# Optimization experiments

Measured on AMD Instinct MI355X. Metric: run time of the kernel, lower is better.

## Reference

```python
import jax, jax.numpy as jnp
import numpy as np

B, IN_DIM, OUT_DIM, W_DIM, K, H, W = 16, 512, 512, 512, 3, 64, 64
LEAK = 0.2

def setup_inputs() -> dict:
    key = jax.random.key(0)
    ks = jax.random.split(key, 8)
    imgs = jax.random.normal(ks[0], (B, IN_DIM, H, W), dtype=jnp.float32)
    w_embs = jax.random.normal(ks[1], (B, W_DIM), dtype=jnp.float32)
    noise = jax.random.normal(ks[2], (B, 1, H, W), dtype=jnp.float32)
    # learned params (kaiming-ish scaling)
    conv_w = jax.random.normal(ks[3], (OUT_DIM, IN_DIM, K, K), dtype=jnp.float32) / np.sqrt(IN_DIM * K * K)
    conv_b = jax.random.normal(ks[4], (OUT_DIM,), dtype=jnp.float32) * 0.01
    style_w = jax.random.normal(ks[5], (IN_DIM, W_DIM), dtype=jnp.float32) / np.sqrt(W_DIM)
    style_b = jax.random.normal(ks[6], (IN_DIM,), dtype=jnp.float32) * 0.01
    noise_weight = jnp.float32(0.1)
    return {"imgs": imgs, "w_embs": w_embs, "noise": noise,
            "conv_w": conv_w, "conv_b": conv_b,
            "style_w": style_w, "style_b": style_b,
            "noise_weight": noise_weight}

def reference(imgs, w_embs, noise, conv_w, conv_b, style_w, style_b, noise_weight):
    # style modulation: [b, in_dim], +1 as in the torch code
    style = w_embs @ style_w.T + style_b + 1.0
    # per-sample modulated weight: [b, out, in, ky, kx]
    weight = conv_w[None] * style[:, None, :, None, None]
    # demodulation: L2 norm over (in, ky, kx)
    norm = jnp.sqrt(jnp.sum(weight * weight, axis=(2, 3, 4), keepdims=True))
    weight = weight / norm
    # grouped conv trick == vmap of per-sample conv with SAME padding
    def conv_one(x, w):  # x: [c,h,w], w: [out,in,ky,kx]
        return jax.lax.conv_general_dilated(
            x[None], w, window_strides=(1, 1), padding='SAME',
            dimension_numbers=('NCHW', 'OIHW', 'NCHW'))[0]
    out = jax.vmap(conv_one)(imgs, weight)  # [b, out, h, w]
    out = out + conv_b[None, :, None, None] + noise * noise_weight
    # LeakyReLU(0.2)
    return jnp.where(out >= 0, out, LEAK * out)
```

## Files before the change

### kernel.cpp

```cpp
#include <hip/hip_runtime.h>
#include <hip/hip_bf16.h>

#define B_    16
#define CI    512
#define CO    512
#define HH    64
#define WW    64
#define NPIX  4096
#define KTAPS 9
#define KTOT  (CI * KTAPS)
#define LEAK  0.2f

#define PY 66
#define PX 66
#define IMGPAD_ELEMS ((size_t)B_ * PY * PX * CI)

typedef __attribute__((ext_vector_type(8))) __bf16  bf16x8;
typedef __attribute__((ext_vector_type(4))) float   floatx4;

__device__ __forceinline__ void load_lds16(const __bf16* g, __bf16* l) {
    __builtin_amdgcn_global_load_lds(
        (const __attribute__((address_space(1))) unsigned int*)g,
        (__attribute__((address_space(3))) unsigned int*)(unsigned int)(uintptr_t)l,
        16, 0, 0);
}


__global__ void style_kernel(const float* __restrict__ w_embs,
                             const float* __restrict__ style_w,
                             const float* __restrict__ style_b,
                             float* __restrict__ style) {
    int b = blockIdx.y;
    int i = blockIdx.x * 256 + threadIdx.x;
    const float4* we = (const float4*)(w_embs + (size_t)b * 512);
    const float4* sw = (const float4*)(style_w + (size_t)i * 512);
    float acc = 0.f;
    #pragma unroll 8
    for (int k = 0; k < 128; ++k) {
        float4 a = we[k], c = sw[k];
        acc += a.x * c.x + a.y * c.y + a.z * c.z + a.w * c.w;
    }
    style[b * 512 + i] = acc + style_b[i] + 1.0f;
}

__global__ void w2_kernel(const float* __restrict__ conv_w, float* __restrict__ w2) {
    int idx = blockIdx.x * 256 + threadIdx.x;
    const float* p = conv_w + (size_t)idx * 9;
    float s = 0.f;
    #pragma unroll
    for (int t = 0; t < 9; ++t) s += p[t] * p[t];
    w2[idx] = s;
}

__global__ void invn_kernel(const float* __restrict__ w2,
                            const float* __restrict__ style,
                            float* __restrict__ invn) {
    __shared__ float st2[512];
    int b = blockIdx.y;
    int o = blockIdx.x * 256 + threadIdx.x;
    for (int i = threadIdx.x; i < 512; i += 256) {
        float s = style[b * 512 + i];
        st2[i] = s * s;
    }
    __syncthreads();
    const float* wr = w2 + (size_t)o * 512;
    float acc = 0.f;
    #pragma unroll 8
    for (int i = 0; i < 512; ++i) acc += wr[i] * st2[i];
    invn[b * 512 + o] = 1.0f / sqrtf(acc);
}

__global__ void wsh_kernel(const float* __restrict__ conv_w,
                           __bf16* __restrict__ wsh) {
    int o = blockIdx.x * 4 + (threadIdx.x >> 6);
    int i0 = (threadIdx.x & 63) * 8;
    const float* p = conv_w + ((size_t)o * 512 + i0) * 9;
    float w[8][9];
    #pragma unroll
    for (int j = 0; j < 8; ++j)
        #pragma unroll
        for (int t = 0; t < 9; ++t) w[j][t] = p[j * 9 + t];
    __bf16* dstB = wsh + (size_t)o * KTOT + i0;
    #pragma unroll
    for (int t = 0; t < 9; ++t) {
        bf16x8 v;
        #pragma unroll
        for (int j = 0; j < 8; ++j) v[j] = (__bf16)w[j][t];
        *(bf16x8*)(dstB + t * 512) = v;
    }
}

__global__ void halo_kernel(__bf16* __restrict__ imgpad) {
    int t = blockIdx.x * 256 + threadIdx.x;
    if (t >= B_ * 260 * 64) return;
    int c8 = t & 63;
    int rest = t >> 6;
    int px = rest % 260;
    int b = rest / 260;
    int y, x;
    if (px < 66)       { y = 0;  x = px; }
    else if (px < 132) { y = 65; x = px - 66; }
    else { int s = px - 132; y = 1 + (s >> 1); x = (s & 1) * 65; }
    float4 z = {0.f, 0.f, 0.f, 0.f};
    *(float4*)&imgpad[(((size_t)b * PY + y) * PX + x) * 512 + c8 * 8] = z;
}

__global__ void imgpad_kernel(const float* __restrict__ imgs,
                              const float* __restrict__ style,
                              __bf16* __restrict__ imgpad) {
    __shared__ float tile[64][65];
    int ic = blockIdx.x, h = blockIdx.y, b = blockIdx.z;
    int t = threadIdx.x;
    int i0 = ic * 64;
    {
        int li = t >> 2;
        int w0 = (t & 3) * 16;
        const float* src = imgs + (((size_t)(b * 512 + i0 + li) * 64 + h) * 64 + w0);
        float4 v0 = ((const float4*)src)[0];
        float4 v1 = ((const float4*)src)[1];
        float4 v2 = ((const float4*)src)[2];
        float4 v3 = ((const float4*)src)[3];
        tile[li][w0 +  0] = v0.x; tile[li][w0 +  1] = v0.y;
        tile[li][w0 +  2] = v0.z; tile[li][w0 +  3] = v0.w;
        tile[li][w0 +  4] = v1.x; tile[li][w0 +  5] = v1.y;
        tile[li][w0 +  6] = v1.z; tile[li][w0 +  7] = v1.w;
        tile[li][w0 +  8] = v2.x; tile[li][w0 +  9] = v2.y;
        tile[li][w0 + 10] = v2.z; tile[li][w0 + 11] = v2.w;
        tile[li][w0 + 12] = v3.x; tile[li][w0 + 13] = v3.y;
        tile[li][w0 + 14] = v3.z; tile[li][w0 + 15] = v3.w;
    }
    __syncthreads();
    {
        int c0 = (t & 7) * 8;
        float st[8];
        #pragma unroll
        for (int j = 0; j < 8; ++j) st[j] = style[b * 512 + i0 + c0 + j];
        #pragma unroll
        for (int g = 0; g < 2; ++g) {
            int w = (t >> 3) + g * 32;
            bf16x8 v;
            #pragma unroll
            for (int j = 0; j < 8; ++j) v[j] = (__bf16)(tile[c0 + j][w] * st[j]);
            __bf16* dst = imgpad + (((size_t)b * PY + (h + 1)) * PX + (w + 1)) * 512 + i0 + c0;
            *(bf16x8*)dst = v;
        }
    }
}


#define BM 256
#define BN 256
#define BK 64
#define NT 72

#define BAR() { __builtin_amdgcn_sched_barrier(0);                            \
                __builtin_amdgcn_s_barrier();                                 \
                __builtin_amdgcn_sched_barrier(0); }

#define RA(PTR, BUFL, MI) (*(const bf16x8*)((PTR) + (BUFL) * 32768 + (MI) * 2048))
#define RB(PTR, BUFL, NI) (*(const bf16x8*)((PTR) + (BUFL) * 32768 + (NI) * 2048))

#define DSTA(BUFL, H, J) (&As[BUFL][(((H) * 128 + (J) * 64) + (wv << 3)) * 64])
#define DSTB(BUFL, H, J) (&Bs[BUFL][(((H) * 128 + (J) * 64) + (wv << 3)) * 64])

#define MFMA_PH(Q)                                                            \
    __builtin_amdgcn_s_setprio(1);                                            \
    _Pragma("unroll") for (int e = 0; e < 2; ++e) {                           \
      _Pragma("unroll") for (int ni = 0; ni < 4; ++ni) {                      \
        acc[2*(Q)+e][ni] = __builtin_amdgcn_mfma_f32_16x16x32_bf16(           \
            af[e][0], bf[ni][0], acc[2*(Q)+e][ni], 0, 0, 0);                  \
        acc[2*(Q)+e][ni] = __builtin_amdgcn_mfma_f32_16x16x32_bf16(           \
            af[e][1], bf[ni][1], acc[2*(Q)+e][ni], 0, 0, 0);                  \
      }                                                                       \
    }                                                                         \
    __builtin_amdgcn_s_setprio(0);

#define TILE(BUF, T, DO_A, DO_B, VME) {                                       \
                          \
    _Pragma("unroll") for (int ni = 0; ni < 4; ++ni) {                        \
        bf[ni][0] = RB(ldsB0, BUF, ni); bf[ni][1] = RB(ldsB1, BUF, ni);       \
    }                                                                         \
    af[0][0] = RA(ldsA0, BUF, 0); af[0][1] = RA(ldsA1, BUF, 0);               \
    af[1][0] = RA(ldsA0, BUF, 1); af[1][1] = RA(ldsA1, BUF, 1);               \
    if (DO_A) { int ka = ((T) + 1) * 64;                                      \
        load_lds16(aG00 + ka, DSTA((BUF) ^ 1, 0, 0));                         \
        load_lds16(aG01 + ka, DSTA((BUF) ^ 1, 0, 1)); }                       \
    MFMA_PH(0)                                                                \
                                        \
    af[0][0] = RA(ldsA0, BUF, 2); af[0][1] = RA(ldsA1, BUF, 2);               \
    af[1][0] = RA(ldsA0, BUF, 3); af[1][1] = RA(ldsA1, BUF, 3);               \
    if (DO_A) { int ka = ((T) + 1) * 64;                                      \
        load_lds16(aG10 + ka, DSTA((BUF) ^ 1, 1, 0));                         \
        load_lds16(aG11 + ka, DSTA((BUF) ^ 1, 1, 1)); }                       \
    MFMA_PH(1)                                                                \
    BAR();                                                \
                                        \
    af[0][0] = RA(ldsA0, BUF, 4); af[0][1] = RA(ldsA1, BUF, 4);               \
    af[1][0] = RA(ldsA0, BUF, 5); af[1][1] = RA(ldsA1, BUF, 5);               \
    int bd2_##BUF = 0; (void)bd2_##BUF;                                       \
    if (DO_B) { int t2 = (T) + 2; int tap2 = t2 >> 3; int ic2 = t2 & 7;       \
        int dy2 = tap2 / 3, dx2 = tap2 - 3 * dy2;                             \
        bd2_##BUF = (dy2 * PX + dx2) * 512 + ic2 * 64;                        \
        load_lds16(bG00 + bd2_##BUF, DSTB(BUF, 0, 0));                        \
        load_lds16(bG01 + bd2_##BUF, DSTB(BUF, 0, 1)); }                      \
    MFMA_PH(2)                                                                \
                         \
    af[0][0] = RA(ldsA0, BUF, 6); af[0][1] = RA(ldsA1, BUF, 6);               \
    af[1][0] = RA(ldsA0, BUF, 7); af[1][1] = RA(ldsA1, BUF, 7);               \
    if (DO_B) {                                                               \
        load_lds16(bG10 + bd2_##BUF, DSTB(BUF, 1, 0));                        \
        load_lds16(bG11 + bd2_##BUF, DSTB(BUF, 1, 1)); }                      \
    MFMA_PH(3)                                                                \
    asm volatile("s_waitcnt vmcnt(" #VME ")" ::: "memory");                   \
    __builtin_amdgcn_sched_barrier(0);                                        \
    BAR();                                                                    \
}

__global__ __launch_bounds__(512, 2) void conv_kernel(
    const __bf16* __restrict__ wsh,
    const __bf16* __restrict__ imgpad,
    const float*  __restrict__ invn,
    const float*  __restrict__ conv_b,
    const float*  __restrict__ noise,
    const float*  __restrict__ nw_p,
    float* __restrict__ out)
{
    __shared__ __attribute__((aligned(16))) __bf16 As[2][BM * BK];
    __shared__ __attribute__((aligned(16))) __bf16 Bs[2][BN * BK];

    const int tid = threadIdx.x;
    const int nt = blockIdx.x, mt = blockIdx.y, b = blockIdx.z;
    const int n0 = nt * BN, m0 = mt * BM;

    const int lane = tid & 63;
    const int wv = tid >> 6;
    const int wmi = wv & 1;
    const int wni = wv >> 1;

    const __bf16* iB = imgpad + (size_t)b * PY * PX * CI;

    const int r0   = (wv << 3) + (lane >> 3);
    const int ks_g = (lane & 7) ^ (lane >> 3);

    const __bf16* aG00 = wsh + (size_t)(m0 +   0 +  0 + r0) * KTOT + ks_g * 8;
    const __bf16* aG01 = wsh + (size_t)(m0 +   0 + 64 + r0) * KTOT + ks_g * 8;
    const __bf16* aG10 = wsh + (size_t)(m0 + 128 +  0 + r0) * KTOT + ks_g * 8;
    const __bf16* aG11 = wsh + (size_t)(m0 + 128 + 64 + r0) * KTOT + ks_g * 8;

    const __bf16* bG00 = iB + ((size_t)(nt * 4 + 0) * PX + r0) * 512 + ks_g * 8;
    const __bf16* bG01 = iB + ((size_t)(nt * 4 + 1) * PX + r0) * 512 + ks_g * 8;
    const __bf16* bG10 = iB + ((size_t)(nt * 4 + 2) * PX + r0) * 512 + ks_g * 8;
    const __bf16* bG11 = iB + ((size_t)(nt * 4 + 3) * PX + r0) * 512 + ks_g * 8;

    const int r16 = lane & 15, q4 = lane >> 4, r7 = lane & 7;
    const int s0 = (q4 ^ r7) << 4;
    const char* ldsA0 = (const char*)&As[0][0] + wmi * 16384 + r16 * 128 + s0;
    const char* ldsA1 = (const char*)&As[0][0] + wmi * 16384 + r16 * 128 + (s0 ^ 64);
    const char* ldsB0 = (const char*)&Bs[0][0] + wni * 8192  + r16 * 128 + s0;
    const char* ldsB1 = (const char*)&Bs[0][0] + wni * 8192  + r16 * 128 + (s0 ^ 64);

    floatx4 acc[8][4];
    #pragma unroll
    for (int mi = 0; mi < 8; ++mi)
        #pragma unroll
        for (int ni = 0; ni < 4; ++ni)
            acc[mi][ni] = (floatx4)(0.f);

    load_lds16(aG00, DSTA(0, 0, 0));
    load_lds16(aG01, DSTA(0, 0, 1));
    load_lds16(aG10, DSTA(0, 1, 0));
    load_lds16(aG11, DSTA(0, 1, 1));
    load_lds16(bG00, DSTB(0, 0, 0));
    load_lds16(bG01, DSTB(0, 0, 1));
    load_lds16(bG10, DSTB(0, 1, 0));
    load_lds16(bG11, DSTB(0, 1, 1));
    load_lds16(bG00 + 64, DSTB(1, 0, 0));
    load_lds16(bG01 + 64, DSTB(1, 0, 1));
    load_lds16(bG10 + 64, DSTB(1, 1, 0));
    load_lds16(bG11 + 64, DSTB(1, 1, 1));
    asm volatile("s_waitcnt vmcnt(4)" ::: "memory");
    __builtin_amdgcn_sched_barrier(0);
    BAR();

    bf16x8 af[2][2];
    bf16x8 bf[4][2];

    #pragma unroll 1
    for (int it = 0; it < 35; ++it) {
        int t0 = it * 2;
        TILE(0, t0,     true, true, 4)
        TILE(1, t0 + 1, true, true, 4)
    }
    TILE(0, 70, true,  false, 0)
    TILE(1, 71, false, false, 0)

    float nwv = nw_p[0];
    #pragma unroll
    for (int ni = 0; ni < 4; ++ni) {
        int col = n0 + wni * 64 + ni * 16 + r16;
        float nz = noise[b * NPIX + col] * nwv;
        #pragma unroll
        for (int mi = 0; mi < 8; ++mi) {
            int rowo = m0 + wmi * 128 + mi * 16 + q4 * 4;
            #pragma unroll
            for (int rr = 0; rr < 4; ++rr) {
                float sc = invn[b * 512 + rowo + rr];
                float vv = acc[mi][ni][rr] * sc + conv_b[rowo + rr] + nz;
                out[(((size_t)b * CO + rowo + rr) << 12) + col] = vv >= 0.f ? vv : LEAK * vv;
            }
        }
    }
}


extern "C" void kernel_launch(void* const* d_in, const int* in_sizes, int n_in,
                              void* d_out, int out_size, void* d_ws, size_t ws_size,
                              hipStream_t stream) {
    const float* imgs    = (const float*)d_in[0];
    const float* w_embs  = (const float*)d_in[1];
    const float* noise   = (const float*)d_in[2];
    const float* conv_w  = (const float*)d_in[3];
    const float* conv_b  = (const float*)d_in[4];
    const float* style_w = (const float*)d_in[5];
    const float* style_b = (const float*)d_in[6];
    const float* nw      = (const float*)d_in[7];
    float* out = (float*)d_out;

    char* ws = (char*)d_ws;
    size_t off = 0;
    __bf16* wsh = (__bf16*)(ws + off);       off += (size_t)CO * KTOT * 2;
    __bf16* imgpad = (__bf16*)(ws + off);    off += IMGPAD_ELEMS * 2;
    float* style = (float*)(ws + off);       off += (size_t)B_ * CI * 4;
    float* invn  = (float*)(ws + off);       off += (size_t)B_ * CO * 4;
    float* w2    = (float*)(ws + off);       off += (size_t)CO * CI * 4;

    style_kernel<<<dim3(2, B_), 256, 0, stream>>>(w_embs, style_w, style_b, style);
    w2_kernel<<<dim3(1024), 256, 0, stream>>>(conv_w, w2);
    invn_kernel<<<dim3(2, B_), 256, 0, stream>>>(w2, style, invn);
    wsh_kernel<<<dim3(CO / 4), 256, 0, stream>>>(conv_w, wsh);
    halo_kernel<<<dim3((B_ * 260 * 64 + 255) / 256), 256, 0, stream>>>(imgpad);
    imgpad_kernel<<<dim3(8, HH, B_), 256, 0, stream>>>(imgs, style, imgpad);
    conv_kernel<<<dim3(NPIX / BN, CO / BM, B_), 512, 0, stream>>>(
        wsh, imgpad, invn, conv_b, noise, nw, out);
}
```

Before: 529.6 us.

## Reorder conv main-loop LDS reads and loads; restructure invn as wave-parallel reduction

The conv kernel tile body is rescheduled. All four A-tile global-to-LDS loads are issued at the start of each tile, with incremented pointers, and A fragments are read into two register sets (afA/afB) so two MFMA phases run back-to-back between barriers. B loads are grouped into one block after the mid-tile barrier. Separately, invn_kernel now uses 16 blocks: each wave computes 8 output channels for all 16 batches, using coalesced float4 reads and shuffle reductions instead of one serial 512-long loop per thread. The extra A fragment registers raise register pressure, which could limit occupancy or cause spills at launch_bounds(512,2).

```diff
diff --git a/kernel.cpp b/kernel.cpp
--- a/kernel.cpp
+++ b/kernel.cpp
@@ -55,19 +55,35 @@
 __global__ void invn_kernel(const float* __restrict__ w2,
                             const float* __restrict__ style,
                             float* __restrict__ invn) {
-    __shared__ float st2[512];
-    int b = blockIdx.y;
-    int o = blockIdx.x * 256 + threadIdx.x;
-    for (int i = threadIdx.x; i < 512; i += 256) {
-        float s = style[b * 512 + i];
-        st2[i] = s * s;
+    __shared__ float st2[16 * 512];
+    int t = threadIdx.x;
+    for (int idx = t * 4; idx < 16 * 512; idx += 256 * 4) {
+        float4 s = *(const float4*)&style[idx];
+        float4 q; q.x = s.x * s.x; q.y = s.y * s.y; q.z = s.z * s.z; q.w = s.w * s.w;
+        *(float4*)&st2[idx] = q;
     }
     __syncthreads();
-    const float* wr = w2 + (size_t)o * 512;
-    float acc = 0.f;
-    #pragma unroll 8
-    for (int i = 0; i < 512; ++i) acc += wr[i] * st2[i];
-    invn[b * 512 + o] = 1.0f / sqrtf(acc);
+    int wv = t >> 6, lane = t & 63;
+    int oBase = blockIdx.x * 32 + wv * 8;
+    #pragma unroll
+    for (int oo = 0; oo < 8; ++oo) {
+        int o = oBase + oo;
+        const float4* wr = (const float4*)(w2 + (size_t)o * 512 + lane * 8);
+        float4 a = wr[0], c = wr[1];
+        float p[16];
+        #pragma unroll
+        for (int b = 0; b < 16; ++b) {
+            const float4* s = (const float4*)&st2[b * 512 + lane * 8];
+            float4 s0 = s[0], s1 = s[1];
+            p[b] = a.x * s0.x + a.y * s0.y + a.z * s0.z + a.w * s0.w
+                 + c.x * s1.x + c.y * s1.y + c.z * s1.z + c.w * s1.w;
+        }
+        #pragma unroll
+        for (int d = 1; d < 64; d <<= 1)
+            #pragma unroll
+            for (int b = 0; b < 16; ++b) p[b] += __shfl_xor(p[b], d);
+        if (lane < 16) invn[lane * 512 + o] = 1.0f / sqrtf(p[lane]);
+    }
 }
 
 __global__ void wsh_kernel(const float* __restrict__ conv_w,
@@ -163,54 +179,49 @@
 #define DSTA(BUFL, H, J) (&As[BUFL][(((H) * 128 + (J) * 64) + (wv << 3)) * 64])
 #define DSTB(BUFL, H, J) (&Bs[BUFL][(((H) * 128 + (J) * 64) + (wv << 3)) * 64])
 
-#define MFMA_PH(Q)                                                            \
+#define MFMA_PH(Q, AF)                                                        \
     __builtin_amdgcn_s_setprio(1);                                            \
     _Pragma("unroll") for (int e = 0; e < 2; ++e) {                           \
       _Pragma("unroll") for (int ni = 0; ni < 4; ++ni) {                      \
         acc[2*(Q)+e][ni] = __builtin_amdgcn_mfma_f32_16x16x32_bf16(           \
-            af[e][0], bf[ni][0], acc[2*(Q)+e][ni], 0, 0, 0);                  \
+            AF[e][0], bf[ni][0], acc[2*(Q)+e][ni], 0, 0, 0);                  \
         acc[2*(Q)+e][ni] = __builtin_amdgcn_mfma_f32_16x16x32_bf16(           \
-            af[e][1], bf[ni][1], acc[2*(Q)+e][ni], 0, 0, 0);                  \
+            AF[e][1], bf[ni][1], acc[2*(Q)+e][ni], 0, 0, 0);                  \
       }                                                                       \
     }                                                                         \
     __builtin_amdgcn_s_setprio(0);
 
 #define TILE(BUF, T, DO_A, DO_B, VME) {                                       \
-                          \
+    if (DO_A) {                                                               \
+        load_lds16(aG00, DSTA((BUF) ^ 1, 0, 0));                              \
+        load_lds16(aG01, DSTA((BUF) ^ 1, 0, 1));                              \
+        load_lds16(aG10, DSTA((BUF) ^ 1, 1, 0));                              \
+        load_lds16(aG11, DSTA((BUF) ^ 1, 1, 1));                              \
+        aG00 += 64; aG01 += 64; aG10 += 64; aG11 += 64;                       \
+    }                                                                         \
     _Pragma("unroll") for (int ni = 0; ni < 4; ++ni) {                        \
         bf[ni][0] = RB(ldsB0, BUF, ni); bf[ni][1] = RB(ldsB1, BUF, ni);       \
     }                                                                         \
-    af[0][0] = RA(ldsA0, BUF, 0); af[0][1] = RA(ldsA1, BUF, 0);               \
-    af[1][0] = RA(ldsA0, BUF, 1); af[1][1] = RA(ldsA1, BUF, 1);               \
-    if (DO_A) { int ka = ((T) + 1) * 64;                                      \
-        load_lds16(aG00 + ka, DSTA((BUF) ^ 1, 0, 0));                         \
-        load_lds16(aG01 + ka, DSTA((BUF) ^ 1, 0, 1)); }                       \
-    MFMA_PH(0)                                                                \
-                                        \
-    af[0][0] = RA(ldsA0, BUF, 2); af[0][1] = RA(ldsA1, BUF, 2);               \
-    af[1][0] = RA(ldsA0, BUF, 3); af[1][1] = RA(ldsA1, BUF, 3);               \
-    if (DO_A) { int ka = ((T) + 1) * 64;                                      \
-        load_lds16(aG10 + ka, DSTA((BUF) ^ 1, 1, 0));                         \
-        load_lds16(aG11 + ka, DSTA((BUF) ^ 1, 1, 1)); }                       \
-    MFMA_PH(1)                                                                \
-    BAR();                                                \
-                                        \
-    af[0][0] = RA(ldsA0, BUF, 4); af[0][1] = RA(ldsA1, BUF, 4);               \
-    af[1][0] = RA(ldsA0, BUF, 5); af[1][1] = RA(ldsA1, BUF, 5);               \
-    int bd2_##BUF = 0; (void)bd2_##BUF;                                       \
+    afA[0][0] = RA(ldsA0, BUF, 0); afA[0][1] = RA(ldsA1, BUF, 0);             \
+    afA[1][0] = RA(ldsA0, BUF, 1); afA[1][1] = RA(ldsA1, BUF, 1);             \
+    afB[0][0] = RA(ldsA0, BUF, 2); afB[0][1] = RA(ldsA1, BUF, 2);             \
+    afB[1][0] = RA(ldsA0, BUF, 3); afB[1][1] = RA(ldsA1, BUF, 3);             \
+    MFMA_PH(0, afA)                                                           \
+    MFMA_PH(1, afB)                                                           \
+    afA[0][0] = RA(ldsA0, BUF, 4); afA[0][1] = RA(ldsA1, BUF, 4);             \
+    afA[1][0] = RA(ldsA0, BUF, 5); afA[1][1] = RA(ldsA1, BUF, 5);             \
+    afB[0][0] = RA(ldsA0, BUF, 6); afB[0][1] = RA(ldsA1, BUF, 6);             \
+    afB[1][0] = RA(ldsA0, BUF, 7); afB[1][1] = RA(ldsA1, BUF, 7);             \
+    BAR();                                             \
     if (DO_B) { int t2 = (T) + 2; int tap2 = t2 >> 3; int ic2 = t2 & 7;       \
         int dy2 = tap2 / 3, dx2 = tap2 - 3 * dy2;                             \
-        bd2_##BUF = (dy2 * PX + dx2) * 512 + ic2 * 64;                        \
-        load_lds16(bG00 + bd2_##BUF, DSTB(BUF, 0, 0));                        \
-        load_lds16(bG01 + bd2_##BUF, DSTB(BUF, 0, 1)); }                      \
-    MFMA_PH(2)                                                                \
-                         \
-    af[0][0] = RA(ldsA0, BUF, 6); af[0][1] = RA(ldsA1, BUF, 6);               \
-    af[1][0] = RA(ldsA0, BUF, 7); af[1][1] = RA(ldsA1, BUF, 7);               \
-    if (DO_B) {                                                               \
-        load_lds16(bG10 + bd2_##BUF, DSTB(BUF, 1, 0));                        \
-        load_lds16(bG11 + bd2_##BUF, DSTB(BUF, 1, 1)); }                      \
-    MFMA_PH(3)                                                                \
+        int bd2 = (dy2 * PX + dx2) * 512 + ic2 * 64;                          \
+        load_lds16(bG00 + bd2, DSTB(BUF, 0, 0));                              \
+        load_lds16(bG01 + bd2, DSTB(BUF, 0, 1));                              \
+        load_lds16(bG10 + bd2, DSTB(BUF, 1, 0));                              \
+        load_lds16(bG11 + bd2, DSTB(BUF, 1, 1)); }                            \
+    MFMA_PH(2, afA)                                                           \
+    MFMA_PH(3, afB)                                                           \
     asm volatile("s_waitcnt vmcnt(" #VME ")" ::: "memory");                   \
     __builtin_amdgcn_sched_barrier(0);                                        \
     BAR();                                                                    \
@@ -270,6 +281,7 @@
     load_lds16(aG01, DSTA(0, 0, 1));
     load_lds16(aG10, DSTA(0, 1, 0));
     load_lds16(aG11, DSTA(0, 1, 1));
+    aG00 += 64; aG01 += 64; aG10 += 64; aG11 += 64;
     load_lds16(bG00, DSTB(0, 0, 0));
     load_lds16(bG01, DSTB(0, 0, 1));
     load_lds16(bG10, DSTB(0, 1, 0));
@@ -282,7 +294,7 @@
     __builtin_amdgcn_sched_barrier(0);
     BAR();
 
-    bf16x8 af[2][2];
+    bf16x8 afA[2][2], afB[2][2];
     bf16x8 bf[4][2];
 
     #pragma unroll 1
@@ -336,7 +348,7 @@
 
     style_kernel<<<dim3(2, B_), 256, 0, stream>>>(w_embs, style_w, style_b, style);
     w2_kernel<<<dim3(1024), 256, 0, stream>>>(conv_w, w2);
-    invn_kernel<<<dim3(2, B_), 256, 0, stream>>>(w2, style, invn);
+    invn_kernel<<<dim3(16), 256, 0, stream>>>(w2, style, invn);
     wsh_kernel<<<dim3(CO / 4), 256, 0, stream>>>(conv_w, wsh);
     halo_kernel<<<dim3((B_ * 260 * 64 + 255) / 256), 256, 0, stream>>>(imgpad);
     imgpad_kernel<<<dim3(8, HH, B_), 256, 0, stream>>>(imgs, style, imgpad);
```

New measurement: 542.5 us. 2.4% more time.
